# Performance work log

Hardware: AMD Instinct MI355X
Metric: run time of the kernel (lower is better)

The kernel has to match this reference:

```python
import jax, jax.numpy as jnp
import numpy as np
import math

B, S, D = 2, 2048, 512
N_BUCKETS = 64
N_HYP = int(math.log2(N_BUCKETS))  # 6


def setup_inputs() -> dict:
    key = jax.random.key(0)
    ks = jax.random.split(key, 6)
    x = jax.random.normal(ks[0], (B, S, D), dtype=jnp.float32)
    # torch.nn.Linear params: weight [out,in], bias [out]
    Wq = jax.random.normal(ks[1], (D, D), dtype=jnp.float32) / jnp.sqrt(D)
    bq = jax.random.normal(ks[2], (D,), dtype=jnp.float32) * 0.01
    Wv = jax.random.normal(ks[3], (D, D), dtype=jnp.float32) / jnp.sqrt(D)
    bv = jax.random.normal(ks[4], (D,), dtype=jnp.float32) * 0.01
    hyperplanes = jax.random.normal(ks[5], (D + 1, N_HYP), dtype=jnp.float32)
    return {"x": x, "Wq": Wq, "bq": bq, "Wv": Wv, "bv": bv, "hyperplanes": hyperplanes}


def _get_buckets(q, hyperplanes):
    # append constant-1 feature: [B,S,D+1]
    qa = jnp.concatenate([q, jnp.ones(q.shape[:2] + (1,), q.dtype)], axis=2)
    proj = jnp.einsum('bse,en->bsn', qa, hyperplanes)
    bits = (proj >= 0).astype(jnp.float32)
    powers = (2.0 ** jnp.arange(N_HYP)).astype(jnp.float32)
    return jnp.einsum('bsn,n->bs', bits, powers)  # [B,S] float bucket ids


def reference(x, Wq, bq, Wv, bv, hyperplanes):
    q = x @ Wq.T + bq
    v = x @ Wv.T + bv
    buckets = _get_buckets(q, hyperplanes)  # [B,S]
    scale = 1.0 / math.sqrt(D)

    def body(acc, i):
        # NOTE: faithful to source: tokens IN bucket i are zeroed (masked_fill
        # with mask = buckets == i), then full dense softmax attention.
        mask = (buckets == i)[..., None]  # [B,S,1]
        qb = jnp.where(mask, 0.0, q)
        vb = jnp.where(mask, 0.0, v)
        att = jax.nn.softmax(jnp.einsum('bsd,btd->bst', qb, qb) * scale, axis=-1)
        return acc + jnp.einsum('bst,btd->bsd', att, vb), None

    init = jnp.zeros_like(x)
    out, _ = jax.lax.scan(body, init, jnp.arange(N_BUCKETS, dtype=jnp.float32))
    return out
```

## Files before the change

### kernel.cpp

```cpp
#include <hip/hip_runtime.h>
#include <math.h>

#define B_ 2
#define S_ 2048
#define D_ 512
#define NB_ 64
#define NH_ 6
#define ROWS (B_*S_)
#define SCALE 0.044194173824159216f

typedef float f32x4 __attribute__((ext_vector_type(4)));
typedef __bf16 bf16v8 __attribute__((ext_vector_type(8)));
typedef short s16x8 __attribute__((ext_vector_type(8)));
typedef unsigned short u16x4 __attribute__((ext_vector_type(4)));

__device__ __forceinline__ float b2f(unsigned short u) {
    unsigned int v = (unsigned int)u << 16;
    float f; __builtin_memcpy(&f, &v, 4); return f;
}
__device__ __forceinline__ unsigned short f2b(float f) {
    unsigned int v; __builtin_memcpy(&v, &f, 4);
    v += 0x7fffu + ((v >> 16) & 1u);
    return (unsigned short)(v >> 16);
}

#define GLOAD16(g, l) __builtin_amdgcn_global_load_lds( \
    (const __attribute__((address_space(1))) unsigned int*)(g), \
    (__attribute__((address_space(3))) unsigned int*)(uintptr_t)(l), 16, 0, 0)

__global__ void prep_kernel(
    const float* __restrict__ x, unsigned short* __restrict__ xh,
    const float* __restrict__ Wq, const float* __restrict__ Wv,
    unsigned short* __restrict__ Wqvh,
    float* __restrict__ Mrow, int* __restrict__ cnt, float* __restrict__ sumVall)
{
    int t = blockIdx.x * 256 + threadIdx.x;
    int stride = gridDim.x * 256;
    for (int i = t; i < ROWS * D_ / 4; i += stride) {
        float4 f = ((const float4*)x)[i];
        u16x4 u = { f2b(f.x), f2b(f.y), f2b(f.z), f2b(f.w) };
        ((u16x4*)xh)[i] = u;
    }
    for (int i = t; i < D_ * D_ / 4; i += stride) {
        float4 f = ((const float4*)Wq)[i];
        u16x4 u = { f2b(f.x), f2b(f.y), f2b(f.z), f2b(f.w) };
        ((u16x4*)Wqvh)[i] = u;
        float4 g = ((const float4*)Wv)[i];
        u16x4 w = { f2b(g.x), f2b(g.y), f2b(g.z), f2b(g.w) };
        ((u16x4*)(Wqvh + (size_t)D_ * D_))[i] = w;
    }
    for (int i = t; i < ROWS; i += stride) Mrow[i] = 0.f;
    for (int i = t; i < B_ * NB_; i += stride) cnt[i] = 0;
    for (int i = t; i < B_ * D_; i += stride) sumVall[i] = 0.f;
}

__global__ __launch_bounds__(256) void mfma_proj(
    const unsigned short* __restrict__ A, const unsigned short* __restrict__ B,
    const float* __restrict__ bq, const float* __restrict__ bv,
    float* __restrict__ MrowRaw, unsigned short* __restrict__ qh,
    float* __restrict__ v)
{
    __shared__ unsigned short Als[128 * 64];
    __shared__ unsigned short Bls[64 * 64];
    const int K = D_, N = 2 * D_;
    int tid = threadIdx.x;
    int w = tid >> 6, l = tid & 63;
    int wr = w >> 1, wc = w & 1;

    int gx = gridDim.x;
    int nwg = gx * gridDim.y;
    int lin = blockIdx.y * gx + blockIdx.x;
    int qq = nwg >> 3;
    int wg = (lin & 7) * qq + (lin >> 3);
    int m0 = (wg / gx) * 128, n0 = (wg % gx) * 64;

    const unsigned short* asrc[4];
    #pragma unroll
    for (int j = 0; j < 4; ++j) {
        int chunk = w * 4 + j;
        int r = chunk * 8 + (l >> 3);
        asrc[j] = A + (size_t)(m0 + r) * K + ((l & 7) ^ (l >> 3)) * 8;
    }
    const unsigned short* bsrc[2];
    #pragma unroll
    for (int j = 0; j < 2; ++j) {
        int chunk = w * 2 + j;
        int r = n0 + chunk * 8 + (l >> 3);
        bsrc[j] = B + (size_t)r * K + ((l & 7) ^ (l >> 3)) * 8;
    }

    f32x4 acc[4][2] = {};
    int rl = l & 15, hi = l >> 4;

    for (int k0 = 0; k0 < K; k0 += 64) {
        #pragma unroll
        for (int j = 0; j < 4; ++j) GLOAD16(asrc[j] + k0, Als + (w * 4 + j) * 512);
        #pragma unroll
        for (int j = 0; j < 2; ++j) GLOAD16(bsrc[j] + k0, Bls + (w * 2 + j) * 512);
        __syncthreads();
        bf16v8 af[4][2], bfr[2][2];
        const char* Ab = (const char*)Als;
        const char* Bb = (const char*)Bls;
        #pragma unroll
        for (int kk = 0; kk < 2; ++kk) {
            int kb = kk * 64 + hi * 16;
            #pragma unroll
            for (int f = 0; f < 4; ++f) {
                int ra = wr * 64 + f * 16 + rl;
                af[f][kk] = *(const bf16v8*)(Ab + ra * 128 + (kb ^ ((ra & 7) << 4)));
            }
            #pragma unroll
            for (int f = 0; f < 2; ++f) {
                int rb = wc * 32 + f * 16 + rl;
                bfr[f][kk] = *(const bf16v8*)(Bb + rb * 128 + (kb ^ ((rb & 7) << 4)));
            }
        }
        #pragma unroll
        for (int fm = 0; fm < 4; ++fm)
            #pragma unroll
            for (int fn = 0; fn < 2; ++fn)
                #pragma unroll
                for (int kk = 0; kk < 2; ++kk)
                    acc[fm][fn] = __builtin_amdgcn_mfma_f32_16x16x32_bf16(
                        af[fm][kk], bfr[fn][kk], acc[fm][fn], 0, 0, 0);
        __syncthreads();
    }

    int colBase = n0 + wc * 32;
    if (colBase < D_) {
        #pragma unroll
        for (int fm = 0; fm < 4; ++fm) {
            float p[4] = {0.f, 0.f, 0.f, 0.f};
            #pragma unroll
            for (int fn = 0; fn < 2; ++fn) {
                int col = colBase + fn * 16 + rl;
                float bs = bq[col];
                #pragma unroll
                for (int r = 0; r < 4; ++r) {
                    int row = m0 + wr * 64 + fm * 16 + hi * 4 + r;
                    float cv = acc[fm][fn][r] + bs;
                    unsigned short h = f2b(cv);
                    qh[(size_t)row * D_ + col] = h;
                    float qb = b2f(h);
                    p[r] = fmaf(qb, qb, p[r]);
                }
            }
            #pragma unroll
            for (int mask = 1; mask < 16; mask <<= 1)
                #pragma unroll
                for (int r = 0; r < 4; ++r) p[r] += __shfl_xor(p[r], mask);
            if (rl == 0) {
                #pragma unroll
                for (int r = 0; r < 4; ++r) {
                    int row = m0 + wr * 64 + fm * 16 + hi * 4 + r;
                    atomicAdd(&MrowRaw[row], p[r]);
                }
            }
        }
    } else {
        #pragma unroll
        for (int fm = 0; fm < 4; ++fm)
            #pragma unroll
            for (int fn = 0; fn < 2; ++fn) {
                int col = colBase + fn * 16 + rl - D_;
                float bs = bv[col];
                #pragma unroll
                for (int r = 0; r < 4; ++r) {
                    int row = m0 + wr * 64 + fm * 16 + hi * 4 + r;
                    v[(size_t)row * D_ + col] = acc[fm][fn][r] + bs;
                }
            }
    }
}

__global__ __launch_bounds__(256) void mfma_qk(
    const unsigned short* __restrict__ qh, const int* __restrict__ prm,
    const float* __restrict__ Mrow, unsigned short* __restrict__ Eh)
{
    __shared__ unsigned short Als[128 * 64];
    __shared__ unsigned short Bls[128 * 64];
    const int K = D_;
    int tid = threadIdx.x;
    int w = tid >> 6, l = tid & 63;
    int wr = w >> 1, wc = w & 1;
    int zb = blockIdx.z;
    const unsigned short* A = qh + (size_t)zb * S_ * D_;
    prm += (size_t)zb * S_;
    const float* Mb = Mrow + (size_t)zb * S_;
    unsigned short* Eb = Eh + (size_t)zb * S_ * S_;

    int gx = gridDim.x;
    int nwg = gx * gridDim.y;
    int lin = blockIdx.y * gx + blockIdx.x;
    int qq = nwg >> 3;
    int wg = (lin & 7) * qq + (lin >> 3);
    int m0 = (wg / gx) * 128, n0 = (wg % gx) * 128;

    const unsigned short* asrc[4];
    const unsigned short* bsrc[4];
    #pragma unroll
    for (int j = 0; j < 4; ++j) {
        int chunk = w * 4 + j;
        int r = chunk * 8 + (l >> 3);
        int c = ((l & 7) ^ (l >> 3)) * 8;
        asrc[j] = A + (size_t)(m0 + r) * K + c;
        bsrc[j] = A + (size_t)prm[n0 + r] * K + c;
    }

    f32x4 acc[4][4] = {};
    int rl = l & 15, hi = l >> 4;

    for (int k0 = 0; k0 < K; k0 += 64) {
        #pragma unroll
        for (int j = 0; j < 4; ++j) GLOAD16(asrc[j] + k0, Als + (w * 4 + j) * 512);
        #pragma unroll
        for (int j = 0; j < 4; ++j) GLOAD16(bsrc[j] + k0, Bls + (w * 4 + j) * 512);
        __syncthreads();
        bf16v8 af[4][2], bfr[4][2];
        const char* Ab = (const char*)Als;
        const char* Bb = (const char*)Bls;
        #pragma unroll
        for (int kk = 0; kk < 2; ++kk) {
            int kb = kk * 64 + hi * 16;
            #pragma unroll
            for (int f = 0; f < 4; ++f) {
                int ra = wr * 64 + f * 16 + rl;
                af[f][kk] = *(const bf16v8*)(Ab + ra * 128 + (kb ^ ((ra & 7) << 4)));
                int rb = wc * 64 + f * 16 + rl;
                bfr[f][kk] = *(const bf16v8*)(Bb + rb * 128 + (kb ^ ((rb & 7) << 4)));
            }
        }
        #pragma unroll
        for (int fm = 0; fm < 4; ++fm)
            #pragma unroll
            for (int fn = 0; fn < 4; ++fn)
                #pragma unroll
                for (int kk = 0; kk < 2; ++kk)
                    acc[fm][fn] = __builtin_amdgcn_mfma_f32_16x16x32_bf16(
                        af[fm][kk], bfr[fn][kk], acc[fm][fn], 0, 0, 0);
        __syncthreads();
    }

    #pragma unroll
    for (int fm = 0; fm < 4; ++fm) {
        #pragma unroll
        for (int r = 0; r < 4; ++r) {
            int row = m0 + wr * 64 + fm * 16 + hi * 4 + r;
            float m = Mb[row];
            #pragma unroll
            for (int fn = 0; fn < 4; ++fn) {
                int col = n0 + wc * 64 + fn * 16 + rl;
                float ev = __expf(fmaf(acc[fm][fn][r], SCALE, -m));
                Eb[(size_t)row * S_ + col] = f2b(ev);
            }
        }
    }
}

__global__ __launch_bounds__(256) void mfma_pv64(
    const unsigned short* __restrict__ Eh, const unsigned short* __restrict__ vT,
    const float* __restrict__ sumVall, const float* __restrict__ sumVb,
    const int* __restrict__ bucket, float* __restrict__ out)
{
    __shared__ unsigned short Als[64 * 64];
    __shared__ unsigned short Bls[64 * 64];
    int tid = threadIdx.x, w = tid >> 6, l = tid & 63;
    int wr = w >> 1, wc = w & 1, rl = l & 15, hi = l >> 4;
    int zb = blockIdx.z;
    const unsigned short* A  = Eh + (size_t)zb * S_ * S_;
    const unsigned short* Bv = vT + (size_t)zb * D_ * S_;
    const float* sva = sumVall + (size_t)zb * D_;
    const float* svb = sumVb + (size_t)zb * NB_ * D_;
    const int* bkt = bucket + (size_t)zb * S_;
    float* outb = out + (size_t)zb * S_ * D_;

    int lin = blockIdx.y * 8 + blockIdx.x;
    int xcd = lin & 7, rest = lin >> 3;
    int m0 = (((rest >> 3) << 3) | xcd) * 64;
    int n0 = (rest & 7) * 64;

    const unsigned short* asrc[2];
    const unsigned short* bsrc[2];
    #pragma unroll
    for (int j = 0; j < 2; ++j) {
        int chunk = w * 2 + j;
        int r = chunk * 8 + (l >> 3);
        int c = ((l & 7) ^ (l >> 3)) * 8;
        asrc[j] = A  + (size_t)(m0 + r) * S_ + c;
        bsrc[j] = Bv + (size_t)(n0 + r) * S_ + c;
    }

    f32x4 acc[2][2] = {};
    for (int k0 = 0; k0 < S_; k0 += 64) {
        #pragma unroll
        for (int j = 0; j < 2; ++j) GLOAD16(asrc[j] + k0, Als + (w * 2 + j) * 512);
        #pragma unroll
        for (int j = 0; j < 2; ++j) GLOAD16(bsrc[j] + k0, Bls + (w * 2 + j) * 512);
        __syncthreads();
        bf16v8 af[2][2], bfr[2][2];
        const char* Ab = (const char*)Als;
        const char* Bb = (const char*)Bls;
        #pragma unroll
        for (int kk = 0; kk < 2; ++kk) {
            int kb = kk * 64 + hi * 16;
            #pragma unroll
            for (int f = 0; f < 2; ++f) {
                int ra = wr * 32 + f * 16 + rl;
                af[f][kk] = *(const bf16v8*)(Ab + ra * 128 + (kb ^ ((ra & 7) << 4)));
                int rb = wc * 32 + f * 16 + rl;
                bfr[f][kk] = *(const bf16v8*)(Bb + rb * 128 + (kb ^ ((rb & 7) << 4)));
            }
        }
        #pragma unroll
        for (int fm = 0; fm < 2; ++fm)
            #pragma unroll
            for (int fn = 0; fn < 2; ++fn)
                #pragma unroll
                for (int kk = 0; kk < 2; ++kk)
                    acc[fm][fn] = __builtin_amdgcn_mfma_f32_16x16x32_bf16(
                        af[fm][kk], bfr[fn][kk], acc[fm][fn], 0, 0, 0);
        __syncthreads();
    }
    const float invS = 1.0f / (float)S_;
    #pragma unroll
    for (int fm = 0; fm < 2; ++fm)
        #pragma unroll
        for (int fn = 0; fn < 2; ++fn) {
            int col = n0 + wc * 32 + fn * 16 + rl;
            float sa = sva[col];
            #pragma unroll
            for (int r = 0; r < 4; ++r) {
                int row = m0 + wr * 32 + fm * 16 + hi * 4 + r;
                int bm = bkt[row];
                outb[(size_t)row * D_ + col] =
                    acc[fm][fn][r] + (sa - svb[(size_t)bm * D_ + col]) * invS;
            }
        }
}

__global__ __launch_bounds__(256) void transpose_v(
    const float* __restrict__ v, const int* __restrict__ perm,
    unsigned short* __restrict__ vT)
{
    __shared__ float tl[32][33];
    int b = blockIdx.z;
    int d0 = blockIdx.x * 32, s0 = blockIdx.y * 32;
    int tx = threadIdx.x & 31, ty = threadIdx.x >> 5;
    const float* vb = v + (size_t)b * S_ * D_;
    const int* pm = perm + (size_t)b * S_;
    #pragma unroll
    for (int i = 0; i < 4; ++i)
        tl[ty + i * 8][tx] = vb[(size_t)pm[s0 + ty + i * 8] * D_ + d0 + tx];
    __syncthreads();
    unsigned short* vt = vT + (size_t)b * D_ * S_;
    #pragma unroll
    for (int i = 0; i < 4; ++i)
        vt[(size_t)(d0 + ty + i * 8) * S_ + s0 + tx] = f2b(tl[tx][ty + i * 8]);
}

__global__ __launch_bounds__(64) void bucket_kernel(
    const unsigned short* __restrict__ qh, const float* __restrict__ H,
    int* __restrict__ bucket, float* __restrict__ Mrow,
    int* __restrict__ cnt, int* __restrict__ idxl)
{
    int row = blockIdx.x;
    int lane = threadIdx.x;
    const unsigned short* qr = qh + (size_t)row * D_;
    float proj[NH_] = {};
    s16x8 qv8 = *(const s16x8*)(qr + lane * 8);
    #pragma unroll
    for (int i = 0; i < 8; ++i) {
        float qv = b2f((unsigned short)qv8[i]);
        int d = lane * 8 + i;
        #pragma unroll
        for (int n = 0; n < NH_; ++n)
            proj[n] = fmaf(qv, H[d * NH_ + n], proj[n]);
    }
    #pragma unroll
    for (int off = 32; off; off >>= 1) {
        #pragma unroll
        for (int n = 0; n < NH_; ++n) proj[n] += __shfl_down(proj[n], off);
    }
    if (lane == 0) {
        int bk = 0;
        #pragma unroll
        for (int n = 0; n < NH_; ++n) {
            float p = proj[n] + H[D_ * NH_ + n];
            if (p >= 0.f) bk |= (1 << n);
        }
        bucket[row] = bk;
        Mrow[row] = Mrow[row] * SCALE;
        int b = row >> 11, s = row & (S_ - 1);
        int pos = atomicAdd(&cnt[b * NB_ + bk], 1);
        idxl[((size_t)(b * NB_ + bk)) * S_ + pos] = s;
    }
}

__global__ __launch_bounds__(64) void permprefix_kernel(
    const int* __restrict__ cnt, const int* __restrict__ idxl,
    int* __restrict__ off, int* __restrict__ perm, int* __restrict__ p2b)
{
    int b = blockIdx.x;
    int j = threadIdx.x;
    int c = cnt[b * NB_ + j];
    int x = c;
    #pragma unroll
    for (int o = 1; o < 64; o <<= 1) {
        int y = __shfl_up(x, o);
        if (j >= o) x += y;
    }
    int o = x - c;
    off[b * (NB_ + 1) + j] = o;
    if (j == 63) off[b * (NB_ + 1) + 64] = x;
    const int* lst = idxl + ((size_t)(b * NB_ + j)) * S_;
    for (int k = 0; k < c; ++k) {
        perm[(size_t)b * S_ + o + k] = lst[k];
        p2b[(size_t)b * S_ + o + k] = j;
    }
}

__global__ __launch_bounds__(256) void zwgamma_kernel(
    unsigned short* __restrict__ Eh, const int* __restrict__ p2b,
    const int* __restrict__ off, const int* __restrict__ cnt,
    const int* __restrict__ bucket, const float* __restrict__ Mrow)
{
    int row = blockIdx.x;
    int b = row >> 11;
    __shared__ float er[S_];
    __shared__ float zl[NB_];
    __shared__ float wl[NB_ + 1];
    int tid = threadIdx.x;
    unsigned short* Er = Eh + (size_t)row * S_;
    int t0 = tid * 8;
    s16x8 ev = *(const s16x8*)(Er + t0);
    #pragma unroll
    for (int i = 0; i < 8; ++i)
        er[t0 + i] = b2f((unsigned short)ev[i]);
    __syncthreads();
    {
        int j = tid >> 2, sub = tid & 3;
        int lo = off[b * (NB_ + 1) + j], hiX = off[b * (NB_ + 1) + j + 1];
        float z = 0.f;
        for (int k = lo + sub; k < hiX; k += 4) z += er[k];
        z += __shfl_xor(z, 1);
        z += __shfl_xor(z, 2);
        if (sub == 0) zl[j] = z;
    }
    __syncthreads();
    if (tid < NB_) {
        int j = tid;
        float zj = zl[j];
        float ztot = zj;
        #pragma unroll
        for (int o = 32; o; o >>= 1) ztot += __shfl_xor(ztot, o);
        int bs = bucket[row];
        float em = __expf(-Mrow[row]);
        float wj = 0.f;
        if (j != bs) wj = 1.0f / (ztot - zj + (float)cnt[b * NB_ + j] * em);
        float Wt = wj;
        #pragma unroll
        for (int o = 32; o; o >>= 1) Wt += __shfl_xor(Wt, o);
        wl[j] = wj;
        if (j == 0) wl[NB_] = Wt;
    }
    __syncthreads();
    float Wt = wl[NB_];
    const int* pb = p2b + (size_t)b * S_ + t0;
    int4 b0 = *(const int4*)pb;
    int4 b1 = *(const int4*)(pb + 4);
    s16x8 ov;
    ov[0] = (short)f2b(er[t0 + 0] * (Wt - wl[b0.x]));
    ov[1] = (short)f2b(er[t0 + 1] * (Wt - wl[b0.y]));
    ov[2] = (short)f2b(er[t0 + 2] * (Wt - wl[b0.z]));
    ov[3] = (short)f2b(er[t0 + 3] * (Wt - wl[b0.w]));
    ov[4] = (short)f2b(er[t0 + 4] * (Wt - wl[b1.x]));
    ov[5] = (short)f2b(er[t0 + 5] * (Wt - wl[b1.y]));
    ov[6] = (short)f2b(er[t0 + 6] * (Wt - wl[b1.z]));
    ov[7] = (short)f2b(er[t0 + 7] * (Wt - wl[b1.w]));
    *(s16x8*)(Er + t0) = ov;
}

__global__ __launch_bounds__(256) void sumv2_kernel(
    const float* __restrict__ v, const int* __restrict__ cnt,
    const int* __restrict__ idxl, float* __restrict__ sumVb,
    float* __restrict__ sumVall)
{
    int j = blockIdx.x, b = blockIdx.y;
    int d = blockIdx.z * 256 + threadIdx.x;
    int n = cnt[b * NB_ + j];
    const int* lst = idxl + ((size_t)(b * NB_ + j)) * S_;
    const float* vb = v + (size_t)b * S_ * D_;
    float acc = 0.f;
    for (int k = 0; k < n; ++k)
        acc += vb[(size_t)lst[k] * D_ + d];
    sumVb[((size_t)b * NB_ + j) * D_ + d] = acc;
    atomicAdd(&sumVall[b * D_ + d], acc);
}

extern "C" void kernel_launch(void* const* d_in, const int* in_sizes, int n_in,
                              void* d_out, int out_size, void* d_ws, size_t ws_size,
                              hipStream_t stream) {
    (void)in_sizes; (void)n_in; (void)out_size; (void)ws_size;
    const float* x  = (const float*)d_in[0];
    const float* Wq = (const float*)d_in[1];
    const float* bq = (const float*)d_in[2];
    const float* Wv = (const float*)d_in[3];
    const float* bv = (const float*)d_in[4];
    const float* H  = (const float*)d_in[5];
    float* out = (float*)d_out;

    char* p = (char*)d_ws;
    auto alloc = [&](size_t bytes) -> char* {
        char* r = p; p += (bytes + 255) & ~(size_t)255; return r;
    };
    float* v       = (float*)alloc((size_t)ROWS * D_ * 4);
    float* Mrow    = (float*)alloc((size_t)ROWS * 4);
    float* sumVb   = (float*)alloc((size_t)B_ * NB_ * D_ * 4);
    float* sumVall = (float*)alloc((size_t)B_ * D_ * 4);
    int*   bucket  = (int*)alloc((size_t)ROWS * 4);
    int*   cnt     = (int*)alloc((size_t)B_ * NB_ * 4);
    int*   offb    = (int*)alloc((size_t)B_ * (NB_ + 1) * 4);
    int*   perm    = (int*)alloc((size_t)B_ * S_ * 4);
    int*   p2b     = (int*)alloc((size_t)B_ * S_ * 4);
    int*   idxl    = (int*)alloc((size_t)B_ * NB_ * S_ * 4);
    unsigned short* xh   = (unsigned short*)alloc((size_t)ROWS * D_ * 2);
    unsigned short* qh   = (unsigned short*)alloc((size_t)ROWS * D_ * 2);
    unsigned short* Wqvh = (unsigned short*)alloc((size_t)2 * D_ * D_ * 2);
    unsigned short* vTh  = (unsigned short*)alloc((size_t)B_ * D_ * S_ * 2);
    unsigned short* Eh   = (unsigned short*)alloc((size_t)B_ * S_ * S_ * 2);

    prep_kernel<<<2048, 256, 0, stream>>>(x, xh, Wq, Wv, Wqvh, Mrow, cnt, sumVall);
    mfma_proj<<<dim3(2 * D_ / 64, ROWS / 128, 1), 256, 0, stream>>>(
        xh, Wqvh, bq, bv, Mrow, qh, v);
    bucket_kernel<<<ROWS, 64, 0, stream>>>(qh, H, bucket, Mrow, cnt, idxl);
    permprefix_kernel<<<B_, 64, 0, stream>>>(cnt, idxl, offb, perm, p2b);
    sumv2_kernel<<<dim3(NB_, B_, D_ / 256), 256, 0, stream>>>(v, cnt, idxl, sumVb, sumVall);
    transpose_v<<<dim3(D_ / 32, S_ / 32, B_), 256, 0, stream>>>(v, perm, vTh);
    mfma_qk<<<dim3(S_ / 128, S_ / 128, B_), 256, 0, stream>>>(qh, perm, Mrow, Eh);
    zwgamma_kernel<<<ROWS, 256, 0, stream>>>(Eh, p2b, offb, cnt, bucket, Mrow);
    mfma_pv64<<<dim3(D_ / 64, S_ / 64, B_), 256, 0, stream>>>(
        Eh, vTh, sumVall, sumVb, bucket, out);
}
```

Baseline: 111.3 us.

## Split PV GEMM along K with atomic accumulation and merge V prep kernels

The PV GEMM grid is doubled by splitting the 2048-long reduction into two halves, with each half atomically adding into an output that prep_kernel now zeroes. The bucket correction term is added only by the first half. Separately, the V transpose and per-bucket V-sum kernels are merged into one launch to save a launch and let the two run concurrently. The cost is extra atomic traffic on the output, extra zeroing writes, and a nondeterministic summation order.

```diff
diff --git a/kernel.cpp b/kernel.cpp
--- a/kernel.cpp
+++ b/kernel.cpp
@@ -32,7 +32,8 @@
     const float* __restrict__ x, unsigned short* __restrict__ xh,
     const float* __restrict__ Wq, const float* __restrict__ Wv,
     unsigned short* __restrict__ Wqvh,
-    float* __restrict__ Mrow, int* __restrict__ cnt, float* __restrict__ sumVall)
+    float* __restrict__ Mrow, int* __restrict__ cnt, float* __restrict__ sumVall,
+    float* __restrict__ out)
 {
     int t = blockIdx.x * 256 + threadIdx.x;
     int stride = gridDim.x * 256;
@@ -40,6 +41,8 @@
         float4 f = ((const float4*)x)[i];
         u16x4 u = { f2b(f.x), f2b(f.y), f2b(f.z), f2b(f.w) };
         ((u16x4*)xh)[i] = u;
+        float4 z = {0.f, 0.f, 0.f, 0.f};
+        ((float4*)out)[i] = z;
     }
     for (int i = t; i < D_ * D_ / 4; i += stride) {
         float4 f = ((const float4*)Wq)[i];
@@ -62,7 +65,7 @@
 {
     __shared__ unsigned short Als[128 * 64];
     __shared__ unsigned short Bls[64 * 64];
-    const int K = D_, N = 2 * D_;
+    const int K = D_;
     int tid = threadIdx.x;
     int w = tid >> 6, l = tid & 63;
     int wr = w >> 1, wc = w & 1;
@@ -266,7 +269,7 @@
     __shared__ unsigned short Bls[64 * 64];
     int tid = threadIdx.x, w = tid >> 6, l = tid & 63;
     int wr = w >> 1, wc = w & 1, rl = l & 15, hi = l >> 4;
-    int zb = blockIdx.z;
+    int zb = blockIdx.z >> 1, kz = blockIdx.z & 1;
     const unsigned short* A  = Eh + (size_t)zb * S_ * S_;
     const unsigned short* Bv = vT + (size_t)zb * D_ * S_;
     const float* sva = sumVall + (size_t)zb * D_;
@@ -291,7 +294,8 @@
     }
 
     f32x4 acc[2][2] = {};
-    for (int k0 = 0; k0 < S_; k0 += 64) {
+    int kbeg = kz * (S_ / 2), kend = kbeg + S_ / 2;
+    for (int k0 = kbeg; k0 < kend; k0 += 64) {
         #pragma unroll
         for (int j = 0; j < 2; ++j) GLOAD16(asrc[j] + k0, Als + (w * 2 + j) * 512);
         #pragma unroll
@@ -331,31 +335,52 @@
             #pragma unroll
             for (int r = 0; r < 4; ++r) {
                 int row = m0 + wr * 32 + fm * 16 + hi * 4 + r;
-                int bm = bkt[row];
-                outb[(size_t)row * D_ + col] =
-                    acc[fm][fn][r] + (sa - svb[(size_t)bm * D_ + col]) * invS;
-            }
-        }
-}
-
-__global__ __launch_bounds__(256) void transpose_v(
+                float val = acc[fm][fn][r];
+                if (kz == 0) {
+                    int bm = bkt[row];
+                    val += (sa - svb[(size_t)bm * D_ + col]) * invS;
+                }
+                atomicAdd(&outb[(size_t)row * D_ + col], val);
+            }
+        }
+}
+
+__global__ __launch_bounds__(256) void vprep_kernel(
     const float* __restrict__ v, const int* __restrict__ perm,
-    unsigned short* __restrict__ vT)
-{
-    __shared__ float tl[32][33];
-    int b = blockIdx.z;
-    int d0 = blockIdx.x * 32, s0 = blockIdx.y * 32;
-    int tx = threadIdx.x & 31, ty = threadIdx.x >> 5;
-    const float* vb = v + (size_t)b * S_ * D_;
-    const int* pm = perm + (size_t)b * S_;
-    #pragma unroll
-    for (int i = 0; i < 4; ++i)
-        tl[ty + i * 8][tx] = vb[(size_t)pm[s0 + ty + i * 8] * D_ + d0 + tx];
-    __syncthreads();
-    unsigned short* vt = vT + (size_t)b * D_ * S_;
-    #pragma unroll
-    for (int i = 0; i < 4; ++i)
-        vt[(size_t)(d0 + ty + i * 8) * S_ + s0 + tx] = f2b(tl[tx][ty + i * 8]);
+    unsigned short* __restrict__ vT,
+    const int* __restrict__ cnt, const int* __restrict__ idxl,
+    float* __restrict__ sumVb, float* __restrict__ sumVall)
+{
+    int bid = blockIdx.x;
+    if (bid < 2048) {
+        __shared__ float tl[32][33];
+        int b = bid >> 10;
+        int r = bid & 1023;
+        int d0 = (r & 15) * 32, s0 = (r >> 4) * 32;
+        int tx = threadIdx.x & 31, ty = threadIdx.x >> 5;
+        const float* vb = v + (size_t)b * S_ * D_;
+        const int* pm = perm + (size_t)b * S_;
+        #pragma unroll
+        for (int i = 0; i < 4; ++i)
+            tl[ty + i * 8][tx] = vb[(size_t)pm[s0 + ty + i * 8] * D_ + d0 + tx];
+        __syncthreads();
+        unsigned short* vt = vT + (size_t)b * D_ * S_;
+        #pragma unroll
+        for (int i = 0; i < 4; ++i)
+            vt[(size_t)(d0 + ty + i * 8) * S_ + s0 + tx] = f2b(tl[tx][ty + i * 8]);
+    } else {
+        int sid = bid - 2048;
+        int j = sid & 63, b = (sid >> 6) & 1, dblk = sid >> 7;
+        int d = dblk * 256 + threadIdx.x;
+        int n = cnt[b * NB_ + j];
+        const int* lst = idxl + ((size_t)(b * NB_ + j)) * S_;
+        const float* vb = v + (size_t)b * S_ * D_;
+        float acc = 0.f;
+        for (int k = 0; k < n; ++k)
+            acc += vb[(size_t)lst[k] * D_ + d];
+        sumVb[((size_t)b * NB_ + j) * D_ + d] = acc;
+        atomicAdd(&sumVall[b * D_ + d], acc);
+    }
 }
 
 __global__ __launch_bounds__(64) void bucket_kernel(
@@ -478,23 +503,6 @@
     ov[6] = (short)f2b(er[t0 + 6] * (Wt - wl[b1.z]));
     ov[7] = (short)f2b(er[t0 + 7] * (Wt - wl[b1.w]));
     *(s16x8*)(Er + t0) = ov;
-}
-
-__global__ __launch_bounds__(256) void sumv2_kernel(
-    const float* __restrict__ v, const int* __restrict__ cnt,
-    const int* __restrict__ idxl, float* __restrict__ sumVb,
-    float* __restrict__ sumVall)
-{
-    int j = blockIdx.x, b = blockIdx.y;
-    int d = blockIdx.z * 256 + threadIdx.x;
-    int n = cnt[b * NB_ + j];
-    const int* lst = idxl + ((size_t)(b * NB_ + j)) * S_;
-    const float* vb = v + (size_t)b * S_ * D_;
-    float acc = 0.f;
-    for (int k = 0; k < n; ++k)
-        acc += vb[(size_t)lst[k] * D_ + d];
-    sumVb[((size_t)b * NB_ + j) * D_ + d] = acc;
-    atomicAdd(&sumVall[b * D_ + d], acc);
 }
 
 extern "C" void kernel_launch(void* const* d_in, const int* in_sizes, int n_in,
@@ -529,15 +537,14 @@
     unsigned short* vTh  = (unsigned short*)alloc((size_t)B_ * D_ * S_ * 2);
     unsigned short* Eh   = (unsigned short*)alloc((size_t)B_ * S_ * S_ * 2);
 
-    prep_kernel<<<2048, 256, 0, stream>>>(x, xh, Wq, Wv, Wqvh, Mrow, cnt, sumVall);
+    prep_kernel<<<2048, 256, 0, stream>>>(x, xh, Wq, Wv, Wqvh, Mrow, cnt, sumVall, out);
     mfma_proj<<<dim3(2 * D_ / 64, ROWS / 128, 1), 256, 0, stream>>>(
         xh, Wqvh, bq, bv, Mrow, qh, v);
     bucket_kernel<<<ROWS, 64, 0, stream>>>(qh, H, bucket, Mrow, cnt, idxl);
     permprefix_kernel<<<B_, 64, 0, stream>>>(cnt, idxl, offb, perm, p2b);
-    sumv2_kernel<<<dim3(NB_, B_, D_ / 256), 256, 0, stream>>>(v, cnt, idxl, sumVb, sumVall);
-    transpose_v<<<dim3(D_ / 32, S_ / 32, B_), 256, 0, stream>>>(v, perm, vTh);
+    vprep_kernel<<<2048 + 256, 256, 0, stream>>>(v, perm, vTh, cnt, idxl, sumVb, sumVall);
     mfma_qk<<<dim3(S_ / 128, S_ / 128, B_), 256, 0, stream>>>(qh, perm, Mrow, Eh);
     zwgamma_kernel<<<ROWS, 256, 0, stream>>>(Eh, p2b, offb, cnt, bucket, Mrow);
-    mfma_pv64<<<dim3(D_ / 64, S_ / 64, B_), 256, 0, stream>>>(
+    mfma_pv64<<<dim3(D_ / 64, S_ / 64, B_ * 2), 256, 0, stream>>>(
         Eh, vTh, sumVall, sumVb, bucket, out);
 }
```

Measured after the change: 117.8 us. +5.8%, slower.
